# Performance work log

Measured on AMD Instinct MI355X. Metric: run time of the kernel, lower is better.

The kernel has to match this reference:

```python
import jax, jax.numpy as jnp
import numpy as np
import math

B, S, D = 2, 2048, 2048
H = 16
HD = D // H          # 128
LAT = 512            # latent_dim


def setup_inputs() -> dict:
    key = jax.random.key(0)
    ks = jax.random.split(key, 8)
    x = jax.random.normal(ks[0], (B, S, D), dtype=jnp.float32)
    freqs = jax.random.uniform(ks[1], (S, HD // 2), dtype=jnp.float32) * (2 * math.pi)
    # additive causal mask: 0 on/below diagonal, -1e9 above
    causal = jnp.tril(jnp.ones((S, S), dtype=bool))
    mask = jnp.where(causal, 0.0, -1e9).astype(jnp.float32)
    sc = 0.02
    Wq = jax.random.normal(ks[2], (D, H * HD), dtype=jnp.float32) * sc
    Wdown = jax.random.normal(ks[3], (D, LAT), dtype=jnp.float32) * sc
    Wkup = jax.random.normal(ks[4], (LAT, H * HD), dtype=jnp.float32) * sc
    Wvup = jax.random.normal(ks[5], (LAT, H * HD), dtype=jnp.float32) * sc
    Wo = jax.random.normal(ks[6], (D, D), dtype=jnp.float32) * sc
    return {"x": x, "freqs": freqs, "mask": mask,
            "Wq": Wq, "Wdown": Wdown, "Wkup": Wkup, "Wvup": Wvup, "Wo": Wo}


def _apply_rope(t, cos, sin):
    # t: [B, S, H, HD]; cos/sin: [1, S, 1, HD//2]
    tp = t.reshape(t.shape[:-1] + (HD // 2, 2))
    t0, t1 = tp[..., 0], tp[..., 1]
    rot = jnp.stack([t0 * cos - t1 * sin, t0 * sin + t1 * cos], axis=-1)
    return rot.reshape(t.shape)


def reference(x, freqs, mask, Wq, Wdown, Wkup, Wvup, Wo):
    b, s, d = x.shape
    Q = (x @ Wq).reshape(b, s, H, HD)
    c_kv = x @ Wdown                       # [B, S, LAT] low-rank latent
    K = (c_kv @ Wkup).reshape(b, s, H, HD)
    V = (c_kv @ Wvup).reshape(b, s, H, HD)
    cos = jnp.cos(freqs)[None, :, None, :]
    sin = jnp.sin(freqs)[None, :, None, :]
    Q = _apply_rope(Q, cos, sin)
    K = _apply_rope(K, cos, sin)
    scores = jnp.einsum('bqhd,bkhd->bhqk', Q, K) / math.sqrt(HD)
    scores = scores + mask                 # [S,S] broadcast over [B,H,S,S]
    probs = jax.nn.softmax(scores, axis=-1)
    attn = jnp.einsum('bhqk,bkhd->bqhd', probs, V).reshape(b, s, d)
    return attn @ Wo
```

## Files before the change

kernel.cpp:

```cpp
#include <hip/hip_runtime.h>
#include <hip/hip_bf16.h>
#include <math.h>

typedef __hip_bfloat16 bf16;
typedef __attribute__((ext_vector_type(8))) short short8;
typedef __attribute__((ext_vector_type(4))) float f32x4;
typedef __attribute__((ext_vector_type(16))) float f32x16;

static constexpr int BB   = 2;
static constexpr int SS   = 2048;
static constexpr int DD   = 2048;
static constexpr int NH   = 16;
static constexpr int HDD  = 128;
static constexpr int LATD = 512;
static constexpr int MR   = BB * SS;
static constexpr int QRS  = DD + LATD;

#if __has_builtin(__builtin_amdgcn_exp2f)
#define EXP2F(x) __builtin_amdgcn_exp2f(x)
#else
#define EXP2F(x) exp2f(x)
#endif

__device__ __forceinline__ void async_cp16(const void* g, void* l) {
    __builtin_amdgcn_global_load_lds(
        (const __attribute__((address_space(1))) void*)g,
        (__attribute__((address_space(3))) void*)l, 16, 0, 0);
}

__device__ __forceinline__ unsigned short bf_bits(bf16 v) {
    union { bf16 b; unsigned short u; } cv; cv.b = v; return cv.u;
}

__global__ __launch_bounds__(256) void prep(
    const float* __restrict__ x, bf16* __restrict__ xb,
    const float* __restrict__ Wq, const float* __restrict__ Wdown,
    const float* __restrict__ Wkup, const float* __restrict__ Wvup,
    bf16* __restrict__ WqdT, bf16* __restrict__ WkvT) {
    __shared__ float tile[32][33];
    const int blk = blockIdx.x, tid = threadIdx.x;
    if (blk < 8192) {
        const int i = blk * 256 + tid;
        float4 v = ((const float4*)x)[i];
        ushort4 o;
        o.x = bf_bits(__float2bfloat16(v.x));
        o.y = bf_bits(__float2bfloat16(v.y));
        o.z = bf_bits(__float2bfloat16(v.z));
        o.w = bf_bits(__float2bfloat16(v.w));
        ((ushort4*)xb)[i] = o;
        return;
    }
    const float* in; bf16* out; int rows, cols, bx, by;
    if (blk < 12288) {
        const int l = blk - 8192;  in = Wq;    out = WqdT;
        rows = DD;   cols = DD;    bx = l & 63; by = l >> 6;
    } else if (blk < 13312) {
        const int l = blk - 12288; in = Wdown; out = WqdT + (size_t)DD * DD;
        rows = DD;   cols = LATD;  bx = l & 15; by = l >> 4;
    } else if (blk < 14336) {
        const int l = blk - 13312; in = Wkup;  out = WkvT;
        rows = LATD; cols = DD;    bx = l & 63; by = l >> 6;
    } else {
        const int l = blk - 14336; in = Wvup;  out = WkvT + (size_t)DD * LATD;
        rows = LATD; cols = DD;    bx = l & 63; by = l >> 6;
    }
    const int tx = tid & 31, ty = tid >> 5;
    const int c0 = bx * 32, r0 = by * 32;
    for (int i = 0; i < 32; i += 8)
        tile[ty + i][tx] = in[(size_t)(r0 + ty + i) * cols + c0 + tx];
    __syncthreads();
    for (int i = 0; i < 32; i += 8)
        out[(size_t)(c0 + ty + i) * rows + r0 + tx] =
            __float2bfloat16(tile[tx][ty + i]);
}

template <bool OUT_F32, bool ROPE>
__global__ __launch_bounds__(256) void gemm_bt(
    const bf16* __restrict__ A, const bf16* __restrict__ Bt,
    void* __restrict__ Cout, int M, int N, int K, int lda, int ldb, int ldc,
    const float* __restrict__ freqs) {
    __shared__ bf16 As[2][128 * 32];
    __shared__ bf16 Bs[2][128 * 32];
    const int tid  = threadIdx.x;
    const int lane = tid & 63, wave = tid >> 6;
    const int quad = lane >> 4, l16 = lane & 15;

    const int nx = N >> 7, ny = M >> 7;
    const int nwg = nx * ny;
    const int wg  = ((blockIdx.x & 7) * (nwg >> 3)) + (blockIdx.x >> 3);
    const int nig = nx << 3;
    const int brow = ((wg / nig) << 3) + (wg & 7);
    const int bcol = (wg % nig) >> 3;
    const int row0 = brow * 128, col0 = bcol * 128;

    const int wm = (wave >> 1) * 64, wn = (wave & 1) * 64;
    const int srow = lane >> 2;
    const int scol = (lane & 3) * 8;

    f32x4 acc[4][4];
    for (int i = 0; i < 4; ++i)
        for (int j = 0; j < 4; ++j)
            for (int r = 0; r < 4; ++r) acc[i][j][r] = 0.f;

    auto stage = [&](int k0, int bufi) {
        for (int c = 0; c < 2; ++c) {
            const int chunk = wave * 2 + c;
            const int r = chunk * 16 + srow;
            async_cp16(A  + (size_t)(row0 + r) * lda + k0 + scol, &As[bufi][chunk * 512]);
            async_cp16(Bt + (size_t)(col0 + r) * ldb + k0 + scol, &Bs[bufi][chunk * 512]);
        }
    };

    const int nk = K / 32;
    stage(0, 0);
    for (int ki = 0; ki < nk; ++ki) {
        __syncthreads();
        if (ki + 1 < nk) stage((ki + 1) * 32, (ki + 1) & 1);
        const int bi = ki & 1;
        short8 af[4], bfr[4];
        for (int t = 0; t < 4; ++t) {
            af[t]  = *(const short8*)&As[bi][(wm + t * 16 + l16) * 32 + quad * 8];
            bfr[t] = *(const short8*)&Bs[bi][(wn + t * 16 + l16) * 32 + quad * 8];
        }
        for (int i = 0; i < 4; ++i)
            for (int j = 0; j < 4; ++j)
                acc[i][j] = __builtin_amdgcn_mfma_f32_16x16x32_bf16(
                    af[i], bfr[j], acc[i][j], 0, 0, 0);
    }

    const int rbase = row0 + wm + quad * 4;
    const int cbase = col0 + wn + l16;
    if (OUT_F32) {
        float* C = (float*)Cout;
        for (int i = 0; i < 4; ++i)
            for (int j = 0; j < 4; ++j)
                for (int r = 0; r < 4; ++r)
                    C[(size_t)(rbase + i * 16 + r) * ldc + cbase + j * 16] = acc[i][j][r];
    } else if (ROPE && col0 < 2048) {
        bf16* C = (bf16*)Cout;
        for (int i = 0; i < 4; ++i)
            for (int r = 0; r < 4; ++r) {
                const int s = (rbase + i * 16 + r) & (SS - 1);
                const float* fro = freqs + (size_t)s * 64;
                for (int j = 0; j < 4; ++j) {
                    const int d = wn + j * 16 + l16;
                    const float f = fro[d >> 1];
                    const float cs = __cosf(f), sn = __sinf(f);
                    const float v  = acc[i][j][r];
                    const float vp = __shfl_xor(v, 1);
                    const float o  = (l16 & 1) ? (vp * sn + v * cs)
                                               : (v * cs - vp * sn);
                    C[(size_t)(rbase + i * 16 + r) * ldc + cbase + j * 16] =
                        __float2bfloat16(o);
                }
            }
    } else {
        bf16* C = (bf16*)Cout;
        for (int i = 0; i < 4; ++i)
            for (int j = 0; j < 4; ++j)
                for (int r = 0; r < 4; ++r)
                    C[(size_t)(rbase + i * 16 + r) * ldc + cbase + j * 16] =
                        __float2bfloat16(acc[i][j][r]);
    }
}

__global__ __launch_bounds__(256) void tvrope(
    bf16* __restrict__ KV, bf16* __restrict__ VT,
    const float* __restrict__ Wo, bf16* __restrict__ WoT) {
    __shared__ __align__(16) char sm[64 * 74 * 2];
    const int blk = blockIdx.x, tid = threadIdx.x;
    if (blk < 2048) {
        bf16 (*t)[74] = (bf16(*)[74])sm;
        const int bx = blk & 31, byy = (blk >> 5) & 1, bh = blk >> 6;
        const int s0 = bx * 64, d0 = byy * 64;
        const int b = bh >> 4, h = bh & 15;
        const bf16* src = KV + (size_t)b * SS * 4096 + 2048 + h * 128 + d0;
        for (int p = 0; p < 2; ++p) {
            const int s = p * 32 + (tid >> 3), dc = (tid & 7) * 8;
            short8 v = *(const short8*)(src + (size_t)(s0 + s) * 4096 + dc);
            const bf16* ve = (const bf16*)&v;
            for (int e = 0; e < 8; ++e) t[s][dc + e] = ve[e];
        }
        __syncthreads();
        bf16* dst = VT + ((size_t)bh * HDD + d0) * SS + s0;
        for (int p = 0; p < 2; ++p) {
            const int d = p * 32 + (tid >> 3), g = tid & 7;
            short8 v; bf16* ve = (bf16*)&v;
            for (int e = 0; e < 8; ++e) ve[e] = t[g * 8 + e][d];
            const int gp = g ^ (d & 7);
            *(short8*)(dst + (size_t)d * SS + gp * 8) = v;
        }
        return;
    }
    {
        float (*tile)[33] = (float(*)[33])sm;
        const int l = blk - 2048;
        const int bx = l & 63, by = l >> 6;
        const int tx = tid & 31, ty = tid >> 5;
        const int c0 = bx * 32, r0 = by * 32;
        for (int i = 0; i < 32; i += 8)
            tile[ty + i][tx] = Wo[(size_t)(r0 + ty + i) * DD + c0 + tx];
        __syncthreads();
        for (int i = 0; i < 32; i += 8)
            WoT[(size_t)(c0 + ty + i) * DD + r0 + tx] =
                __float2bfloat16(tile[tx][ty + i]);
    }
}

__global__ __launch_bounds__(256, 2) void flash_attn(
    const bf16* __restrict__ QC, const bf16* __restrict__ KV,
    const bf16* __restrict__ VTg, const float* __restrict__ freqs,
    bf16* __restrict__ O) {
    const int j = blockIdx.x;
    const int bh = (j >> 3) & 31, q3 = j & 7;
    const int qt = (j & 256) ? q3 : 15 - q3;
    const int h = bh & (NH - 1), b = bh >> 4;
    const int q0 = qt * 128;
    const int tid = threadIdx.x, lane = tid & 63, wave = tid >> 6;
    const int l32 = lane & 31, hi = lane >> 5;

    __shared__ __align__(16) char smem[66048];
    bf16*  KsB  = (bf16*)smem;
    bf16*  VtB  = (bf16*)(smem + 32768);
    float* RedS = (float*)(smem + 65536);

    const bf16* Kb  = KV  + (size_t)b * SS * 4096 + h * HDD;
    const bf16* VTb = VTg + (size_t)bh * HDD * SS;

    const float QS = 0.08838834764831845f * 1.4426950408889634f;
    const int qrow = q0 + wave * 32 + l32;
    short8 qf[8];
    {
        const bf16* qp = QC + (size_t)(b * SS + qrow) * QRS + h * HDD;
#pragma unroll
        for (int dk = 0; dk < 8; ++dk) {
            short8 v = *(const short8*)(qp + dk * 16 + hi * 8);
            const float4 f = *(const float4*)&freqs[(size_t)qrow * 64 + dk * 8 + hi * 4];
            const float fr[4] = {f.x, f.y, f.z, f.w};
            const bf16* ve = (const bf16*)&v;
            bf16* oe = (bf16*)&qf[dk];
#pragma unroll
            for (int i2 = 0; i2 < 4; ++i2) {
                const float cs = __cosf(fr[i2]), sn = __sinf(fr[i2]);
                const float t0 = __bfloat162float(ve[2 * i2]);
                const float t1 = __bfloat162float(ve[2 * i2 + 1]);
                oe[2 * i2]     = __float2bfloat16((t0 * cs - t1 * sn) * QS);
                oe[2 * i2 + 1] = __float2bfloat16((t0 * sn + t1 * cs) * QS);
            }
        }
    }

    auto stage = [&](int kt, int bufi) {
        const int k0 = kt * 64;
#pragma unroll
        for (int ii = 0; ii < 4; ++ii) {
            const int i = wave * 4 + ii;
            const int krow = 4 * i + (lane >> 4);
            const int csrc = (lane & 15) ^ (krow & 7);
            async_cp16(Kb + (size_t)(k0 + krow) * 4096 + csrc * 8,
                       KsB + bufi * 8192 + i * 512);
            const int d = 8 * i + (lane >> 3);
            async_cp16(VTb + (size_t)d * SS + k0 + (lane & 7) * 8,
                       VtB + bufi * 8192 + i * 512);
        }
    };

    f32x16 accO[4];
#pragma unroll
    for (int d = 0; d < 4; ++d)
#pragma unroll
        for (int r = 0; r < 16; ++r) accO[d][r] = 0.f;
    float m_r = -1e30f, l_r = 0.f;

    const int ktMax = 2 * qt + 1;
    const int qwb = q0 + wave * 32;

    stage(0, 0);
    for (int kt = 0; kt <= ktMax; ++kt) {
        const int k0 = kt * 64;
        __syncthreads();
        if (kt < ktMax) stage(kt + 1, (kt + 1) & 1);
        const int bi = kt & 1;

        if (k0 > qwb + 31) continue;

        f32x16 st[2];
#pragma unroll
        for (int t = 0; t < 2; ++t)
#pragma unroll
            for (int r = 0; r < 16; ++r) st[t][r] = 0.f;
        __builtin_amdgcn_s_setprio(1);
#pragma unroll
        for (int dk = 0; dk < 8; ++dk)
#pragma unroll
            for (int t = 0; t < 2; ++t) {
                const int rd = t * 32 + l32;
                short8 kf = *(const short8*)
                    &KsB[bi * 8192 + rd * 128 + ((((dk << 1) | hi) ^ (rd & 7)) << 3)];
                st[t] = __builtin_amdgcn_mfma_f32_32x32x16_bf16(
                    kf, qf[dk], st[t], 0, 0, 0);
            }
        __builtin_amdgcn_s_setprio(0);

        float p[32];
#pragma unroll
        for (int t = 0; t < 2; ++t)
#pragma unroll
            for (int r = 0; r < 16; ++r) p[t * 16 + r] = st[t][r];

        if (k0 + 63 > qwb) {
#pragma unroll
            for (int t = 0; t < 2; ++t)
#pragma unroll
                for (int r = 0; r < 16; ++r) {
                    const int kv = k0 + t * 32 + (r & 3) + 8 * (r >> 2) + 4 * hi;
                    if (kv > qrow) p[t * 16 + r] = -1e30f;
                }
        }

        float mt[16];
#pragma unroll
        for (int n = 0; n < 16; ++n) mt[n] = fmaxf(p[n], p[n + 16]);
#pragma unroll
        for (int n = 0; n < 8; ++n) mt[n] = fmaxf(mt[n], mt[n + 8]);
#pragma unroll
        for (int n = 0; n < 4; ++n) mt[n] = fmaxf(mt[n], mt[n + 4]);
        float mx = fmaxf(fmaxf(mt[0], mt[1]), fmaxf(mt[2], mt[3]));
        const float rmax = fmaxf(mx, __shfl_xor(mx, 32));

        const bool grow = rmax > m_r + 8.f;
        if (__any(grow)) {
            const float mnew = fmaxf(m_r, rmax);
            const float alpha = EXP2F(m_r - mnew);
            m_r = mnew;
            l_r *= alpha;
            RedS[wave * 32 + l32] = alpha;
            __builtin_amdgcn_s_waitcnt(0xc07f);
#pragma unroll
            for (int r = 0; r < 16; ++r) {
                const float av = RedS[wave * 32 + ((r & 3) + 8 * (r >> 2) + 4 * hi)];
#pragma unroll
                for (int d = 0; d < 4; ++d) accO[d][r] *= av;
            }
        }

#pragma unroll
        for (int r = 0; r < 32; ++r) p[r] = EXP2F(p[r] - m_r);
        float sa[16];
#pragma unroll
        for (int n = 0; n < 16; ++n) sa[n] = p[n] + p[n + 16];
#pragma unroll
        for (int n = 0; n < 8; ++n) sa[n] += sa[n + 8];
#pragma unroll
        for (int n = 0; n < 4; ++n) sa[n] += sa[n + 4];
        float ps = (sa[0] + sa[1]) + (sa[2] + sa[3]);
        l_r += ps + __shfl_xor(ps, 32);

        unsigned int pk[16];
#pragma unroll
        for (int n = 0; n < 16; ++n) {
            const unsigned int lo = bf_bits(__float2bfloat16(p[2 * n]));
            const unsigned int hl = bf_bits(__float2bfloat16(p[2 * n + 1]));
            pk[n] = lo | (hl << 16);
        }

#pragma unroll
        for (int m = 0; m < 4; ++m) {
            const int A0 = 4 * m;
            const unsigned int op0 = __shfl_xor(pk[A0 + 0], 32);
            const unsigned int op1 = __shfl_xor(pk[A0 + 1], 32);
            const unsigned int op2 = __shfl_xor(pk[A0 + 2], 32);
            const unsigned int op3 = __shfl_xor(pk[A0 + 3], 32);
            union { unsigned int w[4]; short8 s; } fr;
            fr.w[0] = hi ? op2 : pk[A0 + 0];
            fr.w[1] = hi ? op3 : pk[A0 + 1];
            fr.w[2] = hi ? pk[A0 + 2] : op0;
            fr.w[3] = hi ? pk[A0 + 3] : op1;
            __builtin_amdgcn_s_setprio(1);
#pragma unroll
            for (int db = 0; db < 4; ++db) {
                const int d = db * 32 + l32;
                short8 vf = *(const short8*)
                    &VtB[bi * 8192 + d * 64 + ((((m << 1) | hi) ^ (d & 7)) << 3)];
                accO[db] = __builtin_amdgcn_mfma_f32_32x32x16_bf16(
                    fr.s, vf, accO[db], 0, 0, 0);
            }
            __builtin_amdgcn_s_setprio(0);
        }
    }

    const float invl = 1.f / l_r;
    RedS[wave * 32 + l32] = invl;
    __builtin_amdgcn_s_waitcnt(0xc07f);
    bf16* Ob = O + (size_t)b * SS * DD + h * HDD;
#pragma unroll
    for (int r = 0; r < 16; ++r) {
        const int row = (r & 3) + 8 * (r >> 2) + 4 * hi;
        const float iv = RedS[wave * 32 + row];
        const size_t ro = (size_t)(q0 + wave * 32 + row) * DD;
#pragma unroll
        for (int db = 0; db < 4; ++db)
            Ob[ro + db * 32 + l32] = __float2bfloat16(accO[db][r] * iv);
    }
}

extern "C" void kernel_launch(void* const* d_in, const int* in_sizes, int n_in,
                              void* d_out, int out_size, void* d_ws, size_t ws_size,
                              hipStream_t stream) {
    (void)in_sizes; (void)n_in; (void)out_size; (void)ws_size;
    const float* x     = (const float*)d_in[0];
    const float* freqs = (const float*)d_in[1];
    const float* Wq    = (const float*)d_in[3];
    const float* Wdown = (const float*)d_in[4];
    const float* Wkup  = (const float*)d_in[5];
    const float* Wvup  = (const float*)d_in[6];
    const float* Wo    = (const float*)d_in[7];
    float* out = (float*)d_out;

    char* ws = (char*)d_ws;
    size_t off = 0;
    auto take = [&](size_t bytes) -> void* {
        void* p = ws + off;
        off += (bytes + 255) & ~(size_t)255;
        return p;
    };
    bf16* xb    = (bf16*)take((size_t)MR * DD * 2);
    bf16* WqdT  = (bf16*)take((size_t)QRS * DD * 2);
    bf16* WkvT  = (bf16*)take((size_t)2 * DD * LATD * 2);
    bf16* QC    = (bf16*)take((size_t)MR * QRS * 2);
    bf16* KVb   = (bf16*)take((size_t)MR * 2 * DD * 2);
    bf16* VTg   = (bf16*)take((size_t)BB * NH * HDD * SS * 2);
    bf16* attn  = xb;
    bf16* WoT   = WqdT;

    prep<<<15360, 256, 0, stream>>>(x, xb, Wq, Wdown, Wkup, Wvup, WqdT, WkvT);

    gemm_bt<false, false><<<(QRS / 128) * (MR / 128), 256, 0, stream>>>(
        xb, WqdT, QC, MR, QRS, DD, DD, DD, QRS, nullptr);
    gemm_bt<false, true><<<(2 * DD / 128) * (MR / 128), 256, 0, stream>>>(
        QC + DD, WkvT, KVb, MR, 2 * DD, LATD, QRS, LATD, 2 * DD, freqs);

    tvrope<<<6144, 256, 0, stream>>>(KVb, VTg, Wo, WoT);

    flash_attn<<<512, 256, 0, stream>>>(QC, KVb, VTg, freqs, attn);

    gemm_bt<true, false><<<(DD / 128) * (MR / 128), 256, 0, stream>>>(
        attn, WoT, out, MR, DD, DD, DD, DD, DD, nullptr);
}
```

Before: 343.7 us.

## Use 256x256-tile 8-wave pipelined GEMM for Q/latent and output projections

Adds a new GEMM kernel with 256x256 output tiles, 512 threads (8 waves), a 64-wide K step, XOR-swizzled LDS and a double-buffered async copy schedule. The copy is split into halves that are interleaved with four MFMA phases under s_setprio. It replaces the 128x128 GEMM for the big x-projection and the final Wo projection, raising data reuse per tile and overlapping loads with compute. The trade-offs are fewer workgroups (e.g. 160 and 128 tiles across the CUs), 128KB of LDS per block, and heavy register use from 32 accumulators per lane, which can limit occupancy.

```diff
diff --git a/kernel.cpp b/kernel.cpp
--- a/kernel.cpp
+++ b/kernel.cpp
@@ -72,6 +72,178 @@
     for (int i = 0; i < 32; i += 8)
         out[(size_t)(c0 + ty + i) * rows + r0 + tx] =
             __float2bfloat16(tile[tx][ty + i]);
+}
+
+template <bool OUT_F32>
+__global__ __launch_bounds__(512) void gemm8p(
+    const bf16* __restrict__ A, const bf16* __restrict__ Bt,
+    void* __restrict__ Cout, int M, int N, int K, int lda, int ldb, int ldc) {
+    __shared__ __align__(16) char smem[131072];
+    const int tid  = threadIdx.x;
+    const int lane = tid & 63, wave = tid >> 6;
+    const int quad = lane >> 4, l16 = lane & 15;
+    const int wm = wave >> 2, wn = wave & 3;
+
+    const int nx = N >> 8, ny = M >> 8;
+    const int nwg = nx * ny;
+    const int wg   = ((blockIdx.x & 7) * (nwg >> 3)) + (blockIdx.x >> 3);
+    const int nig  = nx << 3;
+    const int brow = ((wg / nig) << 3) + (wg & 7);
+    const int bcol = (wg % nig) >> 3;
+    const int row0 = brow << 8, col0 = bcol << 8;
+
+    const int NT = K >> 6;
+
+    auto stageH = [&](int tt, int isB, int h) {
+        char* dst0 = smem + (size_t)((((tt & 1) << 1) | isB) * 32768 + h * 16384)
+                     + tid * 16;
+#pragma unroll
+        for (int l = 0; l < 2; ++l) {
+            const int r  = l * 64 + (tid >> 3);
+            const int gs = (tid & 7) ^ (r & 7);
+            const bf16* src = isB
+                ? Bt + (size_t)(col0 + h * 128 + r) * ldb + tt * 64 + gs * 8
+                : A  + (size_t)(row0 + h * 128 + r) * lda + tt * 64 + gs * 8;
+            async_cp16(src, dst0 + l * 8192);
+        }
+    };
+
+    f32x4 acc[8][4];
+#pragma unroll
+    for (int m = 0; m < 8; ++m)
+#pragma unroll
+        for (int n = 0; n < 4; ++n)
+#pragma unroll
+            for (int r = 0; r < 4; ++r) acc[m][n][r] = 0.f;
+
+    stageH(0, 1, 0); stageH(0, 1, 1); stageH(0, 0, 0); stageH(0, 0, 1);
+    stageH(1, 1, 0); stageH(1, 1, 1);
+    asm volatile("s_waitcnt vmcnt(4)" ::: "memory");
+    __builtin_amdgcn_s_barrier();
+
+    for (int tt = 0; tt < NT; ++tt) {
+        const int pt = tt & 1;
+        const char* Abase = smem + (size_t)((pt << 1) * 32768 + wm * 16384);
+        const char* Bbase = smem + (size_t)(((pt << 1) | 1) * 32768
+                                            + (wn >> 1) * 16384);
+        short8 b01[2][2], b23[2][2], am[4][2];
+
+#pragma unroll
+        for (int n = 0; n < 2; ++n)
+#pragma unroll
+            for (int ks = 0; ks < 2; ++ks) {
+                const int r = ((wn & 1) << 6) + n * 16 + l16;
+                b01[n][ks] = *(const short8*)
+                    (Bbase + r * 128 + ((((ks << 2) | quad) ^ (r & 7)) << 4));
+            }
+#pragma unroll
+        for (int m = 0; m < 4; ++m)
+#pragma unroll
+            for (int ks = 0; ks < 2; ++ks) {
+                const int r = m * 16 + l16;
+                am[m][ks] = *(const short8*)
+                    (Abase + r * 128 + ((((ks << 2) | quad) ^ (r & 7)) << 4));
+            }
+        if (tt + 1 < NT) stageH(tt + 1, 0, 0);
+        __builtin_amdgcn_s_barrier();
+        __builtin_amdgcn_s_waitcnt(0xc07f);
+        __builtin_amdgcn_s_setprio(1);
+#pragma unroll
+        for (int m = 0; m < 4; ++m)
+#pragma unroll
+            for (int n = 0; n < 2; ++n)
+#pragma unroll
+                for (int ks = 0; ks < 2; ++ks)
+                    acc[m][n] = __builtin_amdgcn_mfma_f32_16x16x32_bf16(
+                        am[m][ks], b01[n][ks], acc[m][n], 0, 0, 0);
+        __builtin_amdgcn_s_setprio(0);
+        __builtin_amdgcn_s_barrier();
+
+#pragma unroll
+        for (int n = 0; n < 2; ++n)
+#pragma unroll
+            for (int ks = 0; ks < 2; ++ks) {
+                const int r = ((wn & 1) << 6) + (n + 2) * 16 + l16;
+                b23[n][ks] = *(const short8*)
+                    (Bbase + r * 128 + ((((ks << 2) | quad) ^ (r & 7)) << 4));
+            }
+        if (tt + 1 < NT) stageH(tt + 1, 0, 1);
+        __builtin_amdgcn_s_barrier();
+        __builtin_amdgcn_s_waitcnt(0xc07f);
+        __builtin_amdgcn_s_setprio(1);
+#pragma unroll
+        for (int m = 0; m < 4; ++m)
+#pragma unroll
+            for (int n = 0; n < 2; ++n)
+#pragma unroll
+                for (int ks = 0; ks < 2; ++ks)
+                    acc[m][n + 2] = __builtin_amdgcn_mfma_f32_16x16x32_bf16(
+                        am[m][ks], b23[n][ks], acc[m][n + 2], 0, 0, 0);
+        __builtin_amdgcn_s_setprio(0);
+        __builtin_amdgcn_s_barrier();
+
+#pragma unroll
+        for (int m = 0; m < 4; ++m)
+#pragma unroll
+            for (int ks = 0; ks < 2; ++ks) {
+                const int r = (m + 4) * 16 + l16;
+                am[m][ks] = *(const short8*)
+                    (Abase + r * 128 + ((((ks << 2) | quad) ^ (r & 7)) << 4));
+            }
+        if (tt + 2 < NT) stageH(tt + 2, 1, 0);
+        __builtin_amdgcn_s_barrier();
+        __builtin_amdgcn_s_waitcnt(0xc07f);
+        __builtin_amdgcn_s_setprio(1);
+#pragma unroll
+        for (int m = 0; m < 4; ++m)
+#pragma unroll
+            for (int n = 0; n < 2; ++n)
+#pragma unroll
+                for (int ks = 0; ks < 2; ++ks)
+                    acc[m + 4][n + 2] = __builtin_amdgcn_mfma_f32_16x16x32_bf16(
+                        am[m][ks], b23[n][ks], acc[m + 4][n + 2], 0, 0, 0);
+        __builtin_amdgcn_s_setprio(0);
+        __builtin_amdgcn_s_barrier();
+
+        if (tt + 2 < NT) stageH(tt + 2, 1, 1);
+        __builtin_amdgcn_s_barrier();
+        __builtin_amdgcn_s_setprio(1);
+#pragma unroll
+        for (int m = 0; m < 4; ++m)
+#pragma unroll
+            for (int n = 0; n < 2; ++n)
+#pragma unroll
+                for (int ks = 0; ks < 2; ++ks)
+                    acc[m + 4][n] = __builtin_amdgcn_mfma_f32_16x16x32_bf16(
+                        am[m][ks], b01[n][ks], acc[m + 4][n], 0, 0, 0);
+        __builtin_amdgcn_s_setprio(0);
+        if (tt + 2 < NT) asm volatile("s_waitcnt vmcnt(4)" ::: "memory");
+        else             asm volatile("s_waitcnt vmcnt(0)" ::: "memory");
+        __builtin_amdgcn_s_barrier();
+    }
+
+    const int rbase = row0 + wm * 128 + quad * 4;
+    const int cbase = col0 + wn * 64 + l16;
+    if (OUT_F32) {
+        float* C = (float*)Cout;
+#pragma unroll
+        for (int m = 0; m < 8; ++m)
+#pragma unroll
+            for (int n = 0; n < 4; ++n)
+#pragma unroll
+                for (int r = 0; r < 4; ++r)
+                    C[(size_t)(rbase + m * 16 + r) * ldc + cbase + n * 16] = acc[m][n][r];
+    } else {
+        bf16* C = (bf16*)Cout;
+#pragma unroll
+        for (int m = 0; m < 8; ++m)
+#pragma unroll
+            for (int n = 0; n < 4; ++n)
+#pragma unroll
+                for (int r = 0; r < 4; ++r)
+                    C[(size_t)(rbase + m * 16 + r) * ldc + cbase + n * 16] =
+                        __float2bfloat16(acc[m][n][r]);
+    }
 }
 
 template <bool OUT_F32, bool ROPE>
@@ -435,8 +607,8 @@
 
     prep<<<15360, 256, 0, stream>>>(x, xb, Wq, Wdown, Wkup, Wvup, WqdT, WkvT);
 
-    gemm_bt<false, false><<<(QRS / 128) * (MR / 128), 256, 0, stream>>>(
-        xb, WqdT, QC, MR, QRS, DD, DD, DD, QRS, nullptr);
+    gemm8p<false><<<(QRS / 256) * (MR / 256), 512, 0, stream>>>(
+        xb, WqdT, QC, MR, QRS, DD, DD, DD, QRS);
     gemm_bt<false, true><<<(2 * DD / 128) * (MR / 128), 256, 0, stream>>>(
         QC + DD, WkvT, KVb, MR, 2 * DD, LATD, QRS, LATD, 2 * DD, freqs);
 
@@ -444,6 +616,6 @@
 
     flash_attn<<<512, 256, 0, stream>>>(QC, KVb, VTg, freqs, attn);
 
-    gemm_bt<true, false><<<(DD / 128) * (MR / 128), 256, 0, stream>>>(
-        attn, WoT, out, MR, DD, DD, DD, DD, DD, nullptr);
-}
+    gemm8p<true><<<(DD / 256) * (MR / 256), 512, 0, stream>>>(
+        attn, WoT, out, MR, DD, DD, DD, DD, DD);
+}
```

New measurement: 360.1 us. 4.8% more time.

## Fuse V transpose into KV GEMM epilogue and move Wo transpose into prep

Applied to the files above, without the earlier changes.

The KV up-projection GEMM epilogue now writes V straight into the transposed, swizzled per-head layout that flash attention reads. This removes the separate tvrope kernel and the round trip of V through a row-major buffer. The Wo transpose moves into the prep kernel with its own workspace buffer, and K is now stored with a 2048 stride. The cost is scattered 8-byte stores in the GEMM epilogue instead of coalesced row writes, plus a larger prep launch.

```diff
diff --git a/kernel.cpp b/kernel.cpp
--- a/kernel.cpp
+++ b/kernel.cpp
@@ -36,7 +36,8 @@
     const float* __restrict__ x, bf16* __restrict__ xb,
     const float* __restrict__ Wq, const float* __restrict__ Wdown,
     const float* __restrict__ Wkup, const float* __restrict__ Wvup,
-    bf16* __restrict__ WqdT, bf16* __restrict__ WkvT) {
+    const float* __restrict__ Wo,
+    bf16* __restrict__ WqdT, bf16* __restrict__ WkvT, bf16* __restrict__ WoT) {
     __shared__ float tile[32][33];
     const int blk = blockIdx.x, tid = threadIdx.x;
     if (blk < 8192) {
@@ -60,9 +61,12 @@
     } else if (blk < 14336) {
         const int l = blk - 13312; in = Wkup;  out = WkvT;
         rows = LATD; cols = DD;    bx = l & 63; by = l >> 6;
-    } else {
+    } else if (blk < 15360) {
         const int l = blk - 14336; in = Wvup;  out = WkvT + (size_t)DD * LATD;
         rows = LATD; cols = DD;    bx = l & 63; by = l >> 6;
+    } else {
+        const int l = blk - 15360; in = Wo;    out = WoT;
+        rows = DD;   cols = DD;    bx = l & 63; by = l >> 6;
     }
     const int tx = tid & 31, ty = tid >> 5;
     const int c0 = bx * 32, r0 = by * 32;
@@ -74,11 +78,11 @@
             __float2bfloat16(tile[tx][ty + i]);
 }
 
-template <bool OUT_F32, bool ROPE>
+template <bool OUT_F32, bool KVMODE>
 __global__ __launch_bounds__(256) void gemm_bt(
     const bf16* __restrict__ A, const bf16* __restrict__ Bt,
     void* __restrict__ Cout, int M, int N, int K, int lda, int ldb, int ldc,
-    const float* __restrict__ freqs) {
+    const float* __restrict__ freqs, bf16* __restrict__ VTg) {
     __shared__ bf16 As[2][128 * 32];
     __shared__ bf16 Bs[2][128 * 32];
     const int tid  = threadIdx.x;
@@ -136,7 +140,7 @@
             for (int j = 0; j < 4; ++j)
                 for (int r = 0; r < 4; ++r)
                     C[(size_t)(rbase + i * 16 + r) * ldc + cbase + j * 16] = acc[i][j][r];
-    } else if (ROPE && col0 < 2048) {
+    } else if (KVMODE && col0 < 2048) {
         bf16* C = (bf16*)Cout;
         for (int i = 0; i < 4; ++i)
             for (int r = 0; r < 4; ++r) {
@@ -154,6 +158,24 @@
                         __float2bfloat16(o);
                 }
             }
+    } else if (KVMODE) {
+        const int h = (col0 - 2048) >> 7;
+        const int b = row0 >> 11;
+        bf16* Vt = VTg + (size_t)(b * NH + h) * HDD * SS;
+        for (int i = 0; i < 4; ++i) {
+            const int s4 = (rbase + i * 16) & (SS - 1);
+            const int g  = (s4 >> 3) & 7;
+            const int sb = (s4 & ~63) | (s4 & 7);
+            for (int j = 0; j < 4; ++j) {
+                const int d = wn + j * 16 + l16;
+                ushort4 pv;
+                pv.x = bf_bits(__float2bfloat16(acc[i][j][0]));
+                pv.y = bf_bits(__float2bfloat16(acc[i][j][1]));
+                pv.z = bf_bits(__float2bfloat16(acc[i][j][2]));
+                pv.w = bf_bits(__float2bfloat16(acc[i][j][3]));
+                *(ushort4*)(Vt + (size_t)d * SS + sb + ((g ^ (d & 7)) << 3)) = pv;
+            }
+        }
     } else {
         bf16* C = (bf16*)Cout;
         for (int i = 0; i < 4; ++i)
@@ -161,49 +183,6 @@
                 for (int r = 0; r < 4; ++r)
                     C[(size_t)(rbase + i * 16 + r) * ldc + cbase + j * 16] =
                         __float2bfloat16(acc[i][j][r]);
-    }
-}
-
-__global__ __launch_bounds__(256) void tvrope(
-    bf16* __restrict__ KV, bf16* __restrict__ VT,
-    const float* __restrict__ Wo, bf16* __restrict__ WoT) {
-    __shared__ __align__(16) char sm[64 * 74 * 2];
-    const int blk = blockIdx.x, tid = threadIdx.x;
-    if (blk < 2048) {
-        bf16 (*t)[74] = (bf16(*)[74])sm;
-        const int bx = blk & 31, byy = (blk >> 5) & 1, bh = blk >> 6;
-        const int s0 = bx * 64, d0 = byy * 64;
-        const int b = bh >> 4, h = bh & 15;
-        const bf16* src = KV + (size_t)b * SS * 4096 + 2048 + h * 128 + d0;
-        for (int p = 0; p < 2; ++p) {
-            const int s = p * 32 + (tid >> 3), dc = (tid & 7) * 8;
-            short8 v = *(const short8*)(src + (size_t)(s0 + s) * 4096 + dc);
-            const bf16* ve = (const bf16*)&v;
-            for (int e = 0; e < 8; ++e) t[s][dc + e] = ve[e];
-        }
-        __syncthreads();
-        bf16* dst = VT + ((size_t)bh * HDD + d0) * SS + s0;
-        for (int p = 0; p < 2; ++p) {
-            const int d = p * 32 + (tid >> 3), g = tid & 7;
-            short8 v; bf16* ve = (bf16*)&v;
-            for (int e = 0; e < 8; ++e) ve[e] = t[g * 8 + e][d];
-            const int gp = g ^ (d & 7);
-            *(short8*)(dst + (size_t)d * SS + gp * 8) = v;
-        }
-        return;
-    }
-    {
-        float (*tile)[33] = (float(*)[33])sm;
-        const int l = blk - 2048;
-        const int bx = l & 63, by = l >> 6;
-        const int tx = tid & 31, ty = tid >> 5;
-        const int c0 = bx * 32, r0 = by * 32;
-        for (int i = 0; i < 32; i += 8)
-            tile[ty + i][tx] = Wo[(size_t)(r0 + ty + i) * DD + c0 + tx];
-        __syncthreads();
-        for (int i = 0; i < 32; i += 8)
-            WoT[(size_t)(c0 + ty + i) * DD + r0 + tx] =
-                __float2bfloat16(tile[tx][ty + i]);
     }
 }
 
@@ -224,8 +203,9 @@
     bf16*  VtB  = (bf16*)(smem + 32768);
     float* RedS = (float*)(smem + 65536);
 
-    const bf16* Kb  = KV  + (size_t)b * SS * 4096 + h * HDD;
+    const bf16* Kb  = KV  + (size_t)b * SS * 2048 + h * HDD;
     const bf16* VTb = VTg + (size_t)bh * HDD * SS;
+    const int krs = 2048;
 
     const float QS = 0.08838834764831845f * 1.4426950408889634f;
     const int qrow = q0 + wave * 32 + l32;
@@ -257,7 +237,7 @@
             const int i = wave * 4 + ii;
             const int krow = 4 * i + (lane >> 4);
             const int csrc = (lane & 15) ^ (krow & 7);
-            async_cp16(Kb + (size_t)(k0 + krow) * 4096 + csrc * 8,
+            async_cp16(Kb + (size_t)(k0 + krow) * krs + csrc * 8,
                        KsB + bufi * 8192 + i * 512);
             const int d = 8 * i + (lane >> 3);
             async_cp16(VTb + (size_t)d * SS + k0 + (lane & 7) * 8,
@@ -427,23 +407,22 @@
     bf16* xb    = (bf16*)take((size_t)MR * DD * 2);
     bf16* WqdT  = (bf16*)take((size_t)QRS * DD * 2);
     bf16* WkvT  = (bf16*)take((size_t)2 * DD * LATD * 2);
+    bf16* WoT   = (bf16*)take((size_t)DD * DD * 2);
     bf16* QC    = (bf16*)take((size_t)MR * QRS * 2);
-    bf16* KVb   = (bf16*)take((size_t)MR * 2 * DD * 2);
+    bf16* KVb   = (bf16*)take((size_t)MR * DD * 2);
     bf16* VTg   = (bf16*)take((size_t)BB * NH * HDD * SS * 2);
     bf16* attn  = xb;
-    bf16* WoT   = WqdT;
-
-    prep<<<15360, 256, 0, stream>>>(x, xb, Wq, Wdown, Wkup, Wvup, WqdT, WkvT);
+
+    prep<<<19456, 256, 0, stream>>>(x, xb, Wq, Wdown, Wkup, Wvup, Wo,
+                                    WqdT, WkvT, WoT);
 
     gemm_bt<false, false><<<(QRS / 128) * (MR / 128), 256, 0, stream>>>(
-        xb, WqdT, QC, MR, QRS, DD, DD, DD, QRS, nullptr);
+        xb, WqdT, QC, MR, QRS, DD, DD, DD, QRS, nullptr, nullptr);
     gemm_bt<false, true><<<(2 * DD / 128) * (MR / 128), 256, 0, stream>>>(
-        QC + DD, WkvT, KVb, MR, 2 * DD, LATD, QRS, LATD, 2 * DD, freqs);
-
-    tvrope<<<6144, 256, 0, stream>>>(KVb, VTg, Wo, WoT);
+        QC + DD, WkvT, KVb, MR, 2 * DD, LATD, QRS, LATD, DD, freqs, VTg);
 
     flash_attn<<<512, 256, 0, stream>>>(QC, KVb, VTg, freqs, attn);
 
     gemm_bt<true, false><<<(DD / 128) * (MR / 128), 256, 0, stream>>>(
-        attn, WoT, out, MR, DD, DD, DD, DD, DD, nullptr);
-}
+        attn, WoT, out, MR, DD, DD, DD, DD, DD, nullptr, nullptr);
+}
```

After: 336.8 us. -2.0%, faster.
